# Performance work log

Measured on AMD Instinct MI355X. Metric: run time of the kernel, lower is better.

The kernel has to match this reference:

```python
import jax, jax.numpy as jnp
import numpy as np

L, B, T, D, V = 2, 16, 20, 768, 30000


def setup_inputs() -> dict:
    key = jax.random.key(0)
    k1, k2, k3, k4 = jax.random.split(key, 4)
    answer_embed = jax.random.normal(k1, (L, B, T, D), dtype=jnp.float32)
    vocab_embed = 0.1 * jax.random.normal(k2, (V, D), dtype=jnp.float32)
    # classifier_transform modeled as Linear(D, D): y = x @ W.T + b
    W = jax.random.normal(k3, (D, D), dtype=jnp.float32) * (1.0 / np.sqrt(D))
    b = jax.random.normal(k4, (D,), dtype=jnp.float32) * 0.01
    return {"answer_embed": answer_embed, "vocab_embed": vocab_embed, "W": W, "b": b}


def reference(answer_embed, vocab_embed, W, b):
    # vocab_classifiers: [V, D] after the linear transform
    vocab_classifiers = vocab_embed @ W.T + b
    # Original: broadcast multiply [L,B,T,D,1]*[1,1,1,D,V] then sum over D.
    # Mathematically identical contraction over D -> [L, B, T, V]
    return jnp.einsum('lbtd,vd->lbtv', answer_embed, vocab_classifiers)
```

## Files before the change

kernel.cpp:

```cpp
#include <hip/hip_runtime.h>

#define KDIM 768
#define MANS 640
#define VV   30000
#define NGRP 235

typedef __attribute__((ext_vector_type(4)))  float  f32x4;
typedef __attribute__((ext_vector_type(16))) float  f32x16;
typedef __attribute__((ext_vector_type(8)))  __bf16 bf16x8;

__device__ __forceinline__ unsigned short f2bf(float f) {
    union { float f; unsigned int u; } v; v.f = f;
    unsigned int r = v.u + 0x7fffu + ((v.u >> 16) & 1u);
    return (unsigned short)(r >> 16);
}

__device__ __forceinline__ void load_lds16(const unsigned short* g, unsigned short* l) {
    __builtin_amdgcn_global_load_lds(
        (__attribute__((address_space(1))) void*)(void*)g,
        (__attribute__((address_space(3))) void*)l,
        16, 0, 0);
}

__global__ __launch_bounds__(256) void prep_small(
    const float* __restrict__ W, const float* __restrict__ A,
    const float* __restrict__ b, unsigned short* __restrict__ Wt_bf,
    float* __restrict__ cvec)
{
    __shared__ float ts[64][65];
    const int blk = blockIdx.x;
    if (blk < 144) {
        int bx = (blk % 12) * 64, by = (blk / 12) * 64;
        int tx = threadIdx.x & 63, tg = threadIdx.x >> 6;
#pragma unroll
        for (int i = 0; i < 16; ++i) {
            int r = tg * 16 + i;
            ts[r][tx] = W[(long)(by + r) * KDIM + bx + tx];
        }
        __syncthreads();
#pragma unroll
        for (int i = 0; i < 16; ++i) {
            int r = tg * 16 + i;
            Wt_bf[(long)(bx + r) * KDIM + by + tx] = f2bf(ts[tx][r]);
        }
    } else {
        int row  = (blk - 144) * 4 + (threadIdx.x >> 6);
        int lane = threadIdx.x & 63;
        const float* ap = A + (long)row * KDIM;
        float s = 0.f;
#pragma unroll
        for (int i = 0; i < KDIM / 64; ++i) s += ap[i * 64 + lane] * b[i * 64 + lane];
#pragma unroll
        for (int off = 32; off; off >>= 1) s += __shfl_down(s, off, 64);
        if (lane == 0) cvec[row] = s;
    }
}

__global__ __launch_bounds__(256) void gemm_a2(
    const float* __restrict__ Af, const unsigned short* __restrict__ Bp,
    unsigned short* __restrict__ outp)
{
    constexpr int TM = 64, TN = 128;
    __shared__ unsigned short sA[TM * 64];
    __shared__ unsigned short sB[TN * 64];

    const int t    = threadIdx.x;
    const int lane = t & 63;
    const int w    = t >> 6;
    const int wm   = w >> 1;
    const int wn   = w & 1;
    const int half = lane >> 5;
    const int col  = lane & 31;
    const long m0  = (long)blockIdx.x * TM;
    const long n0  = (long)blockIdx.y * TN;

    f32x16 acc[1][2];
    acc[0][0] = (f32x16)(0.f);
    acc[0][1] = (f32x16)(0.f);

    for (int k0 = 0; k0 < KDIM; k0 += 64) {
#pragma unroll
        for (int j = 0; j < 2; ++j) {
            int s   = (j * 4 + w) * 64 + lane;
            int row = s >> 3;
            int c   = (s & 7) ^ (row & 7);
            const float* g = Af + (m0 + row) * KDIM + k0 + c * 8;
            f32x4 v0 = ((const f32x4*)g)[0], v1 = ((const f32x4*)g)[1];
            ushort4 o0, o1;
            o0.x = f2bf(v0.x); o0.y = f2bf(v0.y); o0.z = f2bf(v0.z); o0.w = f2bf(v0.w);
            o1.x = f2bf(v1.x); o1.y = f2bf(v1.y); o1.z = f2bf(v1.z); o1.w = f2bf(v1.w);
            unsigned short* d = &sA[s * 8];
            ((ushort4*)d)[0] = o0; ((ushort4*)d)[1] = o1;
        }
#pragma unroll
        for (int j = 0; j < 4; ++j) {
            int s   = (j * 4 + w) * 64 + lane;
            int row = s >> 3;
            int c   = (s & 7) ^ (row & 7);
            load_lds16(Bp + (n0 + row) * KDIM + k0 + c * 8,
                       &sB[(j * 4 + w) * 64 * 8]);
        }
        __syncthreads();

#pragma unroll
        for (int g = 0; g < 4; ++g) {
            const int cg = g * 2 + half;
            int arow = wm * 32 + col;
            bf16x8 af = *(const bf16x8*)&sA[(arow * 8 + (cg ^ (arow & 7))) * 8];
#pragma unroll
            for (int fn = 0; fn < 2; ++fn) {
                int brow = wn * 64 + fn * 32 + col;
                bf16x8 bf = *(const bf16x8*)&sB[(brow * 8 + (cg ^ (brow & 7))) * 8];
                acc[0][fn] = __builtin_amdgcn_mfma_f32_32x32x16_bf16(
                    af, bf, acc[0][fn], 0, 0, 0);
            }
        }
        __syncthreads();
    }

#pragma unroll
    for (int fn = 0; fn < 2; ++fn) {
        long n = n0 + wn * 64 + fn * 32 + col;
#pragma unroll
        for (int rg = 0; rg < 16; ++rg) {
            long m = m0 + wm * 32 + (rg & 3) + 8 * (rg >> 2) + 4 * half;
            outp[m * KDIM + n] = f2bf(acc[0][fn][rg]);
        }
    }
}

__global__ __launch_bounds__(256) void gemm_big(
    const unsigned short* __restrict__ A, const float* __restrict__ Bf,
    const float* __restrict__ cvec, float* __restrict__ outp)
{
    const int id    = blockIdx.x;
    const int x     = id & 7;
    const int q     = id >> 3;
    const int m_idx = q % 5;
    const int n_grp = (q / 5) * 8 + x;
    if (n_grp >= NGRP) return;

    __shared__ unsigned short sA[128 * 64];
    __shared__ unsigned short sB[128 * 64];

    const int t    = threadIdx.x;
    const int lane = t & 63;
    const int w    = t >> 6;
    const int wm   = w >> 1;
    const int wn   = w & 1;
    const int half = lane >> 5;
    const int col  = lane & 31;
    const long m0  = (long)m_idx * 128;
    const long n0  = (long)n_grp * 128;

    f32x16 acc[2][2];
#pragma unroll
    for (int i = 0; i < 2; ++i)
#pragma unroll
        for (int j = 0; j < 2; ++j) acc[i][j] = (f32x16)(0.f);

    const unsigned short* ga[4];
    unsigned short*       la[4];
#pragma unroll
    for (int j = 0; j < 4; ++j) {
        int s  = (j * 4 + w) * 64 + lane;
        int row = s >> 3;
        int c   = (s & 7) ^ (row & 7);
        ga[j] = A + (m0 + row) * KDIM + c * 8;
        la[j] = &sA[(j * 4 + w) * 64 * 8];
    }
    const float* gb[4];
    unsigned short* lb[4];
#pragma unroll
    for (int j = 0; j < 4; ++j) {
        int s   = j * 256 + t;
        int row = s >> 3;
        int c   = (s & 7) ^ (row & 7);
        long grow = n0 + row;
        if (grow > VV - 1) grow = VV - 1;
        gb[j] = Bf + grow * KDIM + c * 8;
        lb[j] = &sB[s * 8];
    }

    for (int k0 = 0; k0 < KDIM; k0 += 64) {
#pragma unroll
        for (int j = 0; j < 4; ++j) load_lds16(ga[j] + k0, la[j]);
#pragma unroll
        for (int j = 0; j < 4; ++j) {
            const float* g = gb[j] + k0;
            f32x4 v0 = ((const f32x4*)g)[0], v1 = ((const f32x4*)g)[1];
            ushort4 o0, o1;
            o0.x = f2bf(v0.x); o0.y = f2bf(v0.y); o0.z = f2bf(v0.z); o0.w = f2bf(v0.w);
            o1.x = f2bf(v1.x); o1.y = f2bf(v1.y); o1.z = f2bf(v1.z); o1.w = f2bf(v1.w);
            ((ushort4*)lb[j])[0] = o0; ((ushort4*)lb[j])[1] = o1;
        }
        __syncthreads();

#pragma unroll
        for (int g = 0; g < 4; ++g) {
            const int cg = g * 2 + half;
            bf16x8 af[2], bfr[2];
#pragma unroll
            for (int fm = 0; fm < 2; ++fm) {
                int row = wm * 64 + fm * 32 + col;
                af[fm]  = *(const bf16x8*)&sA[(row * 8 + (cg ^ (row & 7))) * 8];
            }
#pragma unroll
            for (int fn = 0; fn < 2; ++fn) {
                int row = wn * 64 + fn * 32 + col;
                bfr[fn] = *(const bf16x8*)&sB[(row * 8 + (cg ^ (row & 7))) * 8];
            }
#pragma unroll
            for (int fm = 0; fm < 2; ++fm)
#pragma unroll
                for (int fn = 0; fn < 2; ++fn)
                    acc[fm][fn] = __builtin_amdgcn_mfma_f32_32x32x16_bf16(
                        af[fm], bfr[fn], acc[fm][fn], 0, 0, 0);
        }
        __syncthreads();
    }

#pragma unroll
    for (int fm = 0; fm < 2; ++fm)
#pragma unroll
        for (int fn = 0; fn < 2; ++fn) {
            long n = n0 + wn * 64 + fn * 32 + col;
            if (n < VV) {
#pragma unroll
                for (int rg = 0; rg < 16; ++rg) {
                    long m = m0 + wm * 64 + fm * 32
                           + (rg & 3) + 8 * (rg >> 2) + 4 * half;
                    outp[m * (long)VV + n] = acc[fm][fn][rg] + cvec[m];
                }
            }
        }
}

extern "C" void kernel_launch(void* const* d_in, const int* in_sizes, int n_in,
                              void* d_out, int out_size, void* d_ws, size_t ws_size,
                              hipStream_t stream) {
    const float* answer = (const float*)d_in[0];
    const float* vocab  = (const float*)d_in[1];
    const float* W      = (const float*)d_in[2];
    const float* bvec   = (const float*)d_in[3];

    char* ws = (char*)d_ws;
    unsigned short* Wt_bf = (unsigned short*)ws;
    unsigned short* A2_bf = (unsigned short*)(ws + 1179648);
    float*          cptr  = (float*)(ws + 1179648 + 983040);

    prep_small<<<304, 256, 0, stream>>>(W, answer, bvec, Wt_bf, cptr);

    gemm_a2<<<dim3(MANS / 64, KDIM / 128), 256, 0, stream>>>(answer, Wt_bf, A2_bf);

    gemm_big<<<1200, 256, 0, stream>>>(A2_bf, vocab, cptr, (float*)d_out);
}
```

Measured before the change: 231.3 us.

## Replace tiled big GEMM with vocab-strip kernel streaming A from global

The main GEMM changes from 128x128 output tiles with a K-loop staged through LDS to a strip kernel. Each block converts a 32-row slice of the vocab embedding fully into LDS once, then every wave streams rows of the bf16 A matrix directly from global/L2 and covers all 640 rows. This drops the per-K-step barriers and re-staging of A, and reads vocab only once overall. The cost is much more A traffic from L2, only 32-wide N tiles with little register reuse, and 48KB of LDS per block, which may limit occupancy.

```diff
diff --git a/kernel.cpp b/kernel.cpp
--- a/kernel.cpp
+++ b/kernel.cpp
@@ -3,7 +3,8 @@
 #define KDIM 768
 #define MANS 640
 #define VV   30000
-#define NGRP 235
+#define SN   32
+#define NBLK 938
 
 typedef __attribute__((ext_vector_type(4)))  float  f32x4;
 typedef __attribute__((ext_vector_type(16))) float  f32x16;
@@ -74,9 +75,9 @@
     const long m0  = (long)blockIdx.x * TM;
     const long n0  = (long)blockIdx.y * TN;
 
-    f32x16 acc[1][2];
-    acc[0][0] = (f32x16)(0.f);
-    acc[0][1] = (f32x16)(0.f);
+    f32x16 acc[2];
+    acc[0] = (f32x16)(0.f);
+    acc[1] = (f32x16)(0.f);
 
     for (int k0 = 0; k0 < KDIM; k0 += 64) {
 #pragma unroll
@@ -111,8 +112,8 @@
             for (int fn = 0; fn < 2; ++fn) {
                 int brow = wn * 64 + fn * 32 + col;
                 bf16x8 bf = *(const bf16x8*)&sB[(brow * 8 + (cg ^ (brow & 7))) * 8];
-                acc[0][fn] = __builtin_amdgcn_mfma_f32_32x32x16_bf16(
-                    af, bf, acc[0][fn], 0, 0, 0);
+                acc[fn] = __builtin_amdgcn_mfma_f32_32x32x16_bf16(
+                    af, bf, acc[fn], 0, 0, 0);
             }
         }
         __syncthreads();
@@ -124,116 +125,91 @@
 #pragma unroll
         for (int rg = 0; rg < 16; ++rg) {
             long m = m0 + wm * 32 + (rg & 3) + 8 * (rg >> 2) + 4 * half;
-            outp[m * KDIM + n] = f2bf(acc[0][fn][rg]);
-        }
-    }
-}
-
-__global__ __launch_bounds__(256) void gemm_big(
-    const unsigned short* __restrict__ A, const float* __restrict__ Bf,
+            outp[m * KDIM + n] = f2bf(acc[fn][rg]);
+        }
+    }
+}
+
+__global__ __launch_bounds__(256) void gemm_strip(
+    const unsigned short* __restrict__ A2, const float* __restrict__ vocab,
     const float* __restrict__ cvec, float* __restrict__ outp)
 {
-    const int id    = blockIdx.x;
-    const int x     = id & 7;
-    const int q     = id >> 3;
-    const int m_idx = q % 5;
-    const int n_grp = (q / 5) * 8 + x;
-    if (n_grp >= NGRP) return;
-
-    __shared__ unsigned short sA[128 * 64];
-    __shared__ unsigned short sB[128 * 64];
+    __shared__ unsigned short sB[SN * KDIM];
 
     const int t    = threadIdx.x;
     const int lane = t & 63;
     const int w    = t >> 6;
-    const int wm   = w >> 1;
-    const int wn   = w & 1;
+    const int col  = lane & 31;
     const int half = lane >> 5;
-    const int col  = lane & 31;
-    const long m0  = (long)m_idx * 128;
-    const long n0  = (long)n_grp * 128;
-
-    f32x16 acc[2][2];
-#pragma unroll
-    for (int i = 0; i < 2; ++i)
-#pragma unroll
-        for (int j = 0; j < 2; ++j) acc[i][j] = (f32x16)(0.f);
-
-    const unsigned short* ga[4];
-    unsigned short*       la[4];
-#pragma unroll
-    for (int j = 0; j < 4; ++j) {
-        int s  = (j * 4 + w) * 64 + lane;
-        int row = s >> 3;
-        int c   = (s & 7) ^ (row & 7);
-        ga[j] = A + (m0 + row) * KDIM + c * 8;
-        la[j] = &sA[(j * 4 + w) * 64 * 8];
-    }
-    const float* gb[4];
-    unsigned short* lb[4];
-#pragma unroll
-    for (int j = 0; j < 4; ++j) {
-        int s   = j * 256 + t;
-        int row = s >> 3;
-        int c   = (s & 7) ^ (row & 7);
-        long grow = n0 + row;
-        if (grow > VV - 1) grow = VV - 1;
-        gb[j] = Bf + grow * KDIM + c * 8;
-        lb[j] = &sB[s * 8];
-    }
-
-    for (int k0 = 0; k0 < KDIM; k0 += 64) {
-#pragma unroll
-        for (int j = 0; j < 4; ++j) load_lds16(ga[j] + k0, la[j]);
-#pragma unroll
-        for (int j = 0; j < 4; ++j) {
-            const float* g = gb[j] + k0;
+    const long n0  = (long)blockIdx.x * SN;
+
+    {
+        int r  = t >> 3;
+        int cl = t & 7;
+        long grow = n0 + r; if (grow > VV - 1) grow = VV - 1;
+        const float* gp = vocab + grow * KDIM;
+        unsigned short* lrow = sB + r * KDIM;
+#pragma unroll
+        for (int j = 0; j < 12; ++j) {
+            int c = cl + 8 * j;
+            const float* g = gp + c * 8;
             f32x4 v0 = ((const f32x4*)g)[0], v1 = ((const f32x4*)g)[1];
             ushort4 o0, o1;
             o0.x = f2bf(v0.x); o0.y = f2bf(v0.y); o0.z = f2bf(v0.z); o0.w = f2bf(v0.w);
             o1.x = f2bf(v1.x); o1.y = f2bf(v1.y); o1.z = f2bf(v1.z); o1.w = f2bf(v1.w);
-            ((ushort4*)lb[j])[0] = o0; ((ushort4*)lb[j])[1] = o1;
-        }
-        __syncthreads();
-
-#pragma unroll
-        for (int g = 0; g < 4; ++g) {
-            const int cg = g * 2 + half;
-            bf16x8 af[2], bfr[2];
-#pragma unroll
-            for (int fm = 0; fm < 2; ++fm) {
-                int row = wm * 64 + fm * 32 + col;
-                af[fm]  = *(const bf16x8*)&sA[(row * 8 + (cg ^ (row & 7))) * 8];
+            unsigned short* d = lrow + ((c ^ (r & 7)) * 8);
+            ((ushort4*)d)[0] = o0; ((ushort4*)d)[1] = o1;
+        }
+    }
+    __syncthreads();
+
+    const long nout = n0 + col;
+    const bool nok  = (nout < VV);
+
+    const unsigned short* bbase = sB + col * KDIM;
+
+#pragma unroll
+    for (int p = 0; p < 2; ++p) {
+        const long mA = (long)(w + 8 * p) * 32;
+        const long mB = mA + 128;
+        f32x16 accA = (f32x16)(0.f), accB = (f32x16)(0.f);
+        const unsigned short* pa = A2 + (mA + col) * KDIM + half * 8;
+        const unsigned short* pb = A2 + (mB + col) * KDIM + half * 8;
+#pragma unroll 4
+        for (int s = 0; s < 48; ++s) {
+            bf16x8 bf = *(const bf16x8*)(bbase + (((2 * s + half) ^ (col & 7)) * 8));
+            bf16x8 aA = *(const bf16x8*)(pa + s * 16);
+            bf16x8 aB = *(const bf16x8*)(pb + s * 16);
+            accA = __builtin_amdgcn_mfma_f32_32x32x16_bf16(aA, bf, accA, 0, 0, 0);
+            accB = __builtin_amdgcn_mfma_f32_32x32x16_bf16(aB, bf, accB, 0, 0, 0);
+        }
+        if (nok) {
+#pragma unroll
+            for (int rg = 0; rg < 16; ++rg) {
+                long mm = (rg & 3) + 8 * (rg >> 2) + 4 * half;
+                outp[(mA + mm) * (long)VV + nout] = accA[rg] + cvec[mA + mm];
+                outp[(mB + mm) * (long)VV + nout] = accB[rg] + cvec[mB + mm];
             }
-#pragma unroll
-            for (int fn = 0; fn < 2; ++fn) {
-                int row = wn * 64 + fn * 32 + col;
-                bfr[fn] = *(const bf16x8*)&sB[(row * 8 + (cg ^ (row & 7))) * 8];
+        }
+    }
+    {
+        const long mA = (long)(w + 16) * 32;
+        f32x16 acc = (f32x16)(0.f);
+        const unsigned short* pa = A2 + (mA + col) * KDIM + half * 8;
+#pragma unroll 4
+        for (int s = 0; s < 48; ++s) {
+            bf16x8 bf = *(const bf16x8*)(bbase + (((2 * s + half) ^ (col & 7)) * 8));
+            bf16x8 aA = *(const bf16x8*)(pa + s * 16);
+            acc = __builtin_amdgcn_mfma_f32_32x32x16_bf16(aA, bf, acc, 0, 0, 0);
+        }
+        if (nok) {
+#pragma unroll
+            for (int rg = 0; rg < 16; ++rg) {
+                long mm = (rg & 3) + 8 * (rg >> 2) + 4 * half;
+                outp[(mA + mm) * (long)VV + nout] = acc[rg] + cvec[mA + mm];
             }
-#pragma unroll
-            for (int fm = 0; fm < 2; ++fm)
-#pragma unroll
-                for (int fn = 0; fn < 2; ++fn)
-                    acc[fm][fn] = __builtin_amdgcn_mfma_f32_32x32x16_bf16(
-                        af[fm], bfr[fn], acc[fm][fn], 0, 0, 0);
-        }
-        __syncthreads();
-    }
-
-#pragma unroll
-    for (int fm = 0; fm < 2; ++fm)
-#pragma unroll
-        for (int fn = 0; fn < 2; ++fn) {
-            long n = n0 + wn * 64 + fn * 32 + col;
-            if (n < VV) {
-#pragma unroll
-                for (int rg = 0; rg < 16; ++rg) {
-                    long m = m0 + wm * 64 + fm * 32
-                           + (rg & 3) + 8 * (rg >> 2) + 4 * half;
-                    outp[m * (long)VV + n] = acc[fm][fn][rg] + cvec[m];
-                }
-            }
-        }
+        }
+    }
 }
 
 extern "C" void kernel_launch(void* const* d_in, const int* in_sizes, int n_in,
@@ -253,5 +229,5 @@
 
     gemm_a2<<<dim3(MANS / 64, KDIM / 128), 256, 0, stream>>>(answer, Wt_bf, A2_bf);
 
-    gemm_big<<<1200, 256, 0, stream>>>(A2_bf, vocab, cptr, (float*)d_out);
-}
+    gemm_strip<<<NBLK, 256, 0, stream>>>(A2_bf, vocab, cptr, (float*)d_out);
+}
```

Result: slower. 290.1 us (+25.4%).
